# Optimization experiments

Measured on AMD Instinct MI355X. Metric: run time of the kernel, lower is better.

## Reference

```python
import jax, jax.numpy as jnp
import numpy as np

SIZE = 20
DIM = 2 ** SIZE
BATCH = 16
INV_SQRT2 = 1.0 / np.sqrt(2.0).astype(np.float32)

# spec[x] = sum_i (1 - 2*bit_i(x)) for homogeneous z-field (z = ones, zz = {})
_idx = np.arange(DIM, dtype=np.int64)
_popcount = np.zeros(DIM, dtype=np.int64)
for _k in range(SIZE):
    _popcount += (_idx >> _k) & 1
SPEC = jnp.asarray((SIZE - 2 * _popcount).astype(np.float32))  # [DIM]


def _hadamard_all(xr, xi):
    # Apply H on every qubit site sequentially (same math as the gather+sign
    # loop in GateHadamard, expressed as the standard butterfly):
    # for bit=0 slot: (a + b)/sqrt2 ; for bit=1 slot: (a - b)/sqrt2
    B = xr.shape[0]
    for site in range(SIZE):
        lo = 2 ** site
        hi = 2 ** (SIZE - 1 - site)
        xr4 = xr.reshape(B, lo, 2, hi)
        xi4 = xi.reshape(B, lo, 2, hi)
        ar, br = xr4[:, :, 0], xr4[:, :, 1]
        ai, bi = xi4[:, :, 0], xi4[:, :, 1]
        xr = (jnp.stack([ar + br, ar - br], axis=2) * INV_SQRT2).reshape(B, DIM)
        xi = (jnp.stack([ai + bi, ai - bi], axis=2) * INV_SQRT2).reshape(B, DIM)
    return xr, xi


def setup_inputs() -> dict:
    key = jax.random.key(0)
    k1, k2 = jax.random.split(key)
    x_real = jax.random.normal(k1, (BATCH, DIM), dtype=jnp.float32)
    x_imag = jax.random.normal(k2, (BATCH, DIM), dtype=jnp.float32)
    t = jnp.ones((1,), dtype=jnp.float32)
    return {"x_real": x_real, "x_imag": x_imag, "t": t}


def reference(x_real, x_imag, t):
    xr, xi = _hadamard_all(x_real, x_imag)
    # phase multiply: (cos(sp) - i sin(sp)) * (xr + i xi)
    sp = t[0] * SPEC  # [DIM]
    c, s = jnp.cos(sp), jnp.sin(sp)
    yr = c * xr + s * xi
    yi = c * xi - s * xr
    xr, xi = _hadamard_all(yr, yi)
    return jnp.stack([xr, xi])  # [2, BATCH, DIM] (real, imag)
```

## Files before the change

### kernel.cpp

```cpp
#include <hip/hip_runtime.h>
#include <hip/hip_fp16.h>
#include <math.h>

#define DIMN (1 << 20)

typedef unsigned int uint2v __attribute__((ext_vector_type(2)));

__device__ __forceinline__ unsigned int h2u(__half2 v){ union{__half2 h; unsigned int u;} x; x.h=v; return x.u; }
__device__ __forceinline__ __half2 u2h(unsigned int v){ union{unsigned int u; __half2 h;} x; x.u=v; return x.h; }

__device__ __forceinline__ void bf(float& a, float& b) { float s = a + b; b = a - b; a = s; }

template<int CTRL>
__device__ __forceinline__ float dppf(float x) {
    return __int_as_float(__builtin_amdgcn_mov_dpp(__float_as_int(x), CTRL, 0xF, 0xF, true));
}
template<int CTRL>
__device__ __forceinline__ unsigned int dppu(unsigned int x) {
    return (unsigned int)__builtin_amdgcn_mov_dpp((int)x, CTRL, 0xF, 0xF, true);
}
__device__ __forceinline__ float xor4_f(float x) { return dppf<0x1B>(dppf<0x141>(x)); }
__device__ __forceinline__ unsigned int xor4_u(unsigned int x) { return dppu<0x1B>(dppu<0x141>(x)); }

__device__ __forceinline__ float bfly16_f(float x, float sgn) {
#if __has_builtin(__builtin_amdgcn_permlane16_swap)
    uint2v r = __builtin_amdgcn_permlane16_swap(__float_as_uint(x), __float_as_uint(x), false, false);
    return fmaf(sgn, __uint_as_float(r.y), __uint_as_float(r.x));
#else
    float p = __shfl_xor(x, 16);
    return fmaf(sgn, x, p);
#endif
}
__device__ __forceinline__ float bfly32_f(float x, float sgn) {
#if __has_builtin(__builtin_amdgcn_permlane32_swap)
    uint2v r = __builtin_amdgcn_permlane32_swap(__float_as_uint(x), __float_as_uint(x), false, false);
    return fmaf(sgn, __uint_as_float(r.y), __uint_as_float(r.x));
#else
    float p = __shfl_xor(x, 32);
    return fmaf(sgn, x, p);
#endif
}
__device__ __forceinline__ __half2 bfly16_h2(__half2 x, __half2 sgn) {
#if __has_builtin(__builtin_amdgcn_permlane16_swap)
    uint2v r = __builtin_amdgcn_permlane16_swap(h2u(x), h2u(x), false, false);
    return __hfma2(u2h(r.y), sgn, u2h(r.x));
#else
    __half2 p = u2h((unsigned)__shfl_xor((int)h2u(x), 16));
    return __hfma2(x, sgn, p);
#endif
}
__device__ __forceinline__ __half2 bfly32_h2(__half2 x, __half2 sgn) {
#if __has_builtin(__builtin_amdgcn_permlane32_swap)
    uint2v r = __builtin_amdgcn_permlane32_swap(h2u(x), h2u(x), false, false);
    return __hfma2(u2h(r.y), sgn, u2h(r.x));
#else
    __half2 p = u2h((unsigned)__shfl_xor((int)h2u(x), 32));
    return __hfma2(x, sgn, p);
#endif
}

__device__ __forceinline__ void wht16_f32(float v[16], int lane) {
    #pragma unroll
    for (int s = 1; s < 16; s <<= 1)
        #pragma unroll
        for (int r = 0; r < 16; r++)
            if (!(r & s)) bf(v[r], v[r ^ s]);
    {   float sgn = (lane & 1) ? -1.0f : 1.0f;
        #pragma unroll
        for (int r = 0; r < 16; r++) { float p = dppf<0xB1>(v[r]); v[r] = fmaf(sgn, v[r], p); } }
    {   float sgn = (lane & 2) ? -1.0f : 1.0f;
        #pragma unroll
        for (int r = 0; r < 16; r++) { float p = dppf<0x4E>(v[r]); v[r] = fmaf(sgn, v[r], p); } }
    {   float sgn = (lane & 4) ? -1.0f : 1.0f;
        #pragma unroll
        for (int r = 0; r < 16; r++) { float p = xor4_f(v[r]); v[r] = fmaf(sgn, v[r], p); } }
    {   float sgn = (lane & 8) ? -1.0f : 1.0f;
        #pragma unroll
        for (int r = 0; r < 16; r++) { float p = dppf<0x128>(v[r]); v[r] = fmaf(sgn, v[r], p); } }
    {   float sgn = (lane & 16) ? -1.0f : 1.0f;
        #pragma unroll
        for (int r = 0; r < 16; r++) v[r] = bfly16_f(v[r], sgn); }
    {   float sgn = (lane & 32) ? -1.0f : 1.0f;
        #pragma unroll
        for (int r = 0; r < 16; r++) v[r] = bfly32_f(v[r], sgn); }
}

__device__ __forceinline__ void wht16_h2(__half2 v[16], int lane) {
    #pragma unroll
    for (int s = 1; s < 16; s <<= 1)
        #pragma unroll
        for (int r = 0; r < 16; r++)
            if (!(r & s)) {
                __half2 t = __hadd2(v[r], v[r ^ s]);
                v[r ^ s]  = __hsub2(v[r], v[r ^ s]);
                v[r] = t;
            }
    {   __half2 sgn = __float2half2_rn((lane & 1) ? -1.0f : 1.0f);
        #pragma unroll
        for (int r = 0; r < 16; r++) { __half2 p = u2h(dppu<0xB1>(h2u(v[r]))); v[r] = __hfma2(v[r], sgn, p); } }
    {   __half2 sgn = __float2half2_rn((lane & 2) ? -1.0f : 1.0f);
        #pragma unroll
        for (int r = 0; r < 16; r++) { __half2 p = u2h(dppu<0x4E>(h2u(v[r]))); v[r] = __hfma2(v[r], sgn, p); } }
    {   __half2 sgn = __float2half2_rn((lane & 4) ? -1.0f : 1.0f);
        #pragma unroll
        for (int r = 0; r < 16; r++) { __half2 p = u2h(xor4_u(h2u(v[r]))); v[r] = __hfma2(v[r], sgn, p); } }
    {   __half2 sgn = __float2half2_rn((lane & 8) ? -1.0f : 1.0f);
        #pragma unroll
        for (int r = 0; r < 16; r++) { __half2 p = u2h(dppu<0x128>(h2u(v[r]))); v[r] = __hfma2(v[r], sgn, p); } }
    {   __half2 sgn = __float2half2_rn((lane & 16) ? -1.0f : 1.0f);
        #pragma unroll
        for (int r = 0; r < 16; r++) v[r] = bfly16_h2(v[r], sgn); }
    {   __half2 sgn = __float2half2_rn((lane & 32) ? -1.0f : 1.0f);
        #pragma unroll
        for (int r = 0; r < 16; r++) v[r] = bfly32_h2(v[r], sgn); }
}

__device__ __forceinline__ void xorperm8(unsigned int a[8], int m) {
    bool s0 = (m & 1) != 0, s1 = (m & 2) != 0, s2 = (m & 4) != 0;
    unsigned int b0 = s0 ? a[1] : a[0], b1 = s0 ? a[0] : a[1];
    unsigned int b2 = s0 ? a[3] : a[2], b3 = s0 ? a[2] : a[3];
    unsigned int b4 = s0 ? a[5] : a[4], b5 = s0 ? a[4] : a[5];
    unsigned int b6 = s0 ? a[7] : a[6], b7 = s0 ? a[6] : a[7];
    unsigned int c0 = s1 ? b2 : b0, c1 = s1 ? b3 : b1;
    unsigned int c2 = s1 ? b0 : b2, c3 = s1 ? b1 : b3;
    unsigned int c4 = s1 ? b6 : b4, c5 = s1 ? b7 : b5;
    unsigned int c6 = s1 ? b4 : b6, c7 = s1 ? b5 : b7;
    a[0] = s2 ? c4 : c0; a[1] = s2 ? c5 : c1;
    a[2] = s2 ? c6 : c2; a[3] = s2 ? c7 : c3;
    a[4] = s2 ? c0 : c4; a[5] = s2 ? c1 : c5;
    a[6] = s2 ? c2 : c6; a[7] = s2 ? c3 : c7;
}

__global__ __launch_bounds__(256, 4) void p1_kernel(const float* __restrict__ xr,
                                                    const float* __restrict__ xi,
                                                    __half* __restrict__ ws) {
    const int tid = threadIdx.x, lane = tid & 63, w = tid >> 6;
    const int rt = blockIdx.x * 4 + w;
    const float* re = xr + (size_t)rt * 1024;
    const float* im = xi + (size_t)rt * 1024;
    float vr[16], vi[16];
    #pragma unroll
    for (int q = 0; q < 2; q++) {
        const int base = q * 512 + lane * 8;
        float4 a0 = *(const float4*)(re + base);
        float4 a1 = *(const float4*)(re + base + 4);
        float4 b0 = *(const float4*)(im + base);
        float4 b1 = *(const float4*)(im + base + 4);
        vr[q*8+0]=a0.x*0.03125f; vr[q*8+1]=a0.y*0.03125f; vr[q*8+2]=a0.z*0.03125f; vr[q*8+3]=a0.w*0.03125f;
        vr[q*8+4]=a1.x*0.03125f; vr[q*8+5]=a1.y*0.03125f; vr[q*8+6]=a1.z*0.03125f; vr[q*8+7]=a1.w*0.03125f;
        vi[q*8+0]=b0.x*0.03125f; vi[q*8+1]=b0.y*0.03125f; vi[q*8+2]=b0.z*0.03125f; vi[q*8+3]=b0.w*0.03125f;
        vi[q*8+4]=b1.x*0.03125f; vi[q*8+5]=b1.y*0.03125f; vi[q*8+6]=b1.z*0.03125f; vi[q*8+7]=b1.w*0.03125f;
    }
    wht16_f32(vr, lane);
    wht16_f32(vi, lane);
    __half* wr = ws + (size_t)rt * 1024;
    __half* wi = ws + (size_t)16 * DIMN + (size_t)rt * 1024;
    #pragma unroll
    for (int q = 0; q < 2; q++) {
        const int base = q * 512 + lane * 8;
        uint4 pr, pi;
        pr.x = h2u(__floats2half2_rn(vr[q*8+0], vr[q*8+1]));
        pr.y = h2u(__floats2half2_rn(vr[q*8+2], vr[q*8+3]));
        pr.z = h2u(__floats2half2_rn(vr[q*8+4], vr[q*8+5]));
        pr.w = h2u(__floats2half2_rn(vr[q*8+6], vr[q*8+7]));
        pi.x = h2u(__floats2half2_rn(vi[q*8+0], vi[q*8+1]));
        pi.y = h2u(__floats2half2_rn(vi[q*8+2], vi[q*8+3]));
        pi.z = h2u(__floats2half2_rn(vi[q*8+4], vi[q*8+5]));
        pi.w = h2u(__floats2half2_rn(vi[q*8+6], vi[q*8+7]));
        *(uint4*)(wr + base) = pr;
        *(uint4*)(wi + base) = pi;
    }
}

__global__ __launch_bounds__(256, 4) void p3_kernel(const __half* __restrict__ ws,
                                                    float* __restrict__ out) {
    const int tid = threadIdx.x, lane = tid & 63, w = tid >> 6;
    const int rt = blockIdx.x * 4 + w;
    const __half* wr = ws + (size_t)rt * 1024;
    const __half* wi = ws + (size_t)16 * DIMN + (size_t)rt * 1024;
    float vr[16], vi[16];
    #pragma unroll
    for (int q = 0; q < 2; q++) {
        const int base = q * 512 + lane * 8;
        uint4 pr = *(const uint4*)(wr + base);
        uint4 pi = *(const uint4*)(wi + base);
        __half2 a0=u2h(pr.x), a1=u2h(pr.y), a2=u2h(pr.z), a3=u2h(pr.w);
        __half2 b0=u2h(pi.x), b1=u2h(pi.y), b2=u2h(pi.z), b3=u2h(pi.w);
        vr[q*8+0]=__low2float(a0)*0.03125f; vr[q*8+1]=__high2float(a0)*0.03125f;
        vr[q*8+2]=__low2float(a1)*0.03125f; vr[q*8+3]=__high2float(a1)*0.03125f;
        vr[q*8+4]=__low2float(a2)*0.03125f; vr[q*8+5]=__high2float(a2)*0.03125f;
        vr[q*8+6]=__low2float(a3)*0.03125f; vr[q*8+7]=__high2float(a3)*0.03125f;
        vi[q*8+0]=__low2float(b0)*0.03125f; vi[q*8+1]=__high2float(b0)*0.03125f;
        vi[q*8+2]=__low2float(b1)*0.03125f; vi[q*8+3]=__high2float(b1)*0.03125f;
        vi[q*8+4]=__low2float(b2)*0.03125f; vi[q*8+5]=__high2float(b2)*0.03125f;
        vi[q*8+6]=__low2float(b3)*0.03125f; vi[q*8+7]=__high2float(b3)*0.03125f;
    }
    wht16_f32(vr, lane);
    wht16_f32(vi, lane);
    float* outr = out + (size_t)rt * 1024;
    float* outi = out + (size_t)16 * DIMN + (size_t)rt * 1024;
    #pragma unroll
    for (int q = 0; q < 2; q++) {
        const int base = q * 512 + lane * 8;
        *(float4*)(outr + base)     = make_float4(vr[q*8+0], vr[q*8+1], vr[q*8+2], vr[q*8+3]);
        *(float4*)(outr + base + 4) = make_float4(vr[q*8+4], vr[q*8+5], vr[q*8+6], vr[q*8+7]);
        *(float4*)(outi + base)     = make_float4(vi[q*8+0], vi[q*8+1], vi[q*8+2], vi[q*8+3]);
        *(float4*)(outi + base + 4) = make_float4(vi[q*8+4], vi[q*8+5], vi[q*8+6], vi[q*8+7]);
    }
}

__global__ __launch_bounds__(512, 4) void p2_kernel(__half* __restrict__ ws,
                                                    const float* __restrict__ tptr) {
    __shared__ unsigned int tile[1024][16];
    const int tid = threadIdx.x, lane = tid & 63, w = tid >> 6;

    int wg  = blockIdx.x;
    int swz = (wg & 7) * 128 + (wg >> 3);
    const int b  = swz >> 6;
    const int g  = swz & 63;
    const int c0 = g * 16;
    const float tval = tptr[0];

    const int pbase = __popc(lane) + __popc(c0 + w);
    __half2 c2k[6], s2k[6];
    #pragma unroll
    for (int k = 0; k < 6; k++) {
        float ang = tval * (float)(20 - 2 * (pbase + k));
        float s, c;
        __sincosf(ang, &s, &c);
        c2k[k] = __float2half2_rn(c * 0.03125f);
        s2k[k] = __halves2half2(__float2half(s * 0.03125f),
                                __float2half(-s * 0.03125f));
    }

    __half* re = ws + (size_t)b * DIMN + c0;
    __half* im = ws + (size_t)16 * DIMN + (size_t)b * DIMN + c0;

    #pragma unroll
    for (int it = 0; it < 4; it++) {
        int f = it * 512 + tid;
        int h = f >> 1, q = f & 1;
        uint4 ra = *(const uint4*)(re + (size_t)h * 1024 + q * 8);
        uint4 ia = *(const uint4*)(im + (size_t)h * 1024 + q * 8);
        unsigned int w8[8];
        w8[0] = (ra.x & 0xFFFFu) | (ia.x << 16);
        w8[1] = (ra.x >> 16)     | (ia.x & 0xFFFF0000u);
        w8[2] = (ra.y & 0xFFFFu) | (ia.y << 16);
        w8[3] = (ra.y >> 16)     | (ia.y & 0xFFFF0000u);
        w8[4] = (ra.z & 0xFFFFu) | (ia.z << 16);
        w8[5] = (ra.z >> 16)     | (ia.z & 0xFFFF0000u);
        w8[6] = (ra.w & 0xFFFFu) | (ia.w << 16);
        w8[7] = (ra.w >> 16)     | (ia.w & 0xFFFF0000u);
        int e = (h >> 2) & 15;
        xorperm8(w8, e & 7);
        int base = (q * 8) ^ (e & 8);
        *(uint4*)&tile[h][base]     = make_uint4(w8[0], w8[1], w8[2], w8[3]);
        *(uint4*)&tile[h][base + 4] = make_uint4(w8[4], w8[5], w8[6], w8[7]);
    }
    __syncthreads();

    const int e4 = (lane >> 2) & 15;
    const int cp0 = w ^ e4;
    const __half2 sc = __float2half2_rn(0.03125f);
    __half2 v0[16], v1[16];
    #pragma unroll
    for (int r = 0; r < 16; r++) {
        v0[r] = __hmul2(u2h(tile[r * 64 + lane][cp0]),     sc);
        v1[r] = __hmul2(u2h(tile[r * 64 + lane][cp0 ^ 8]), sc);
    }

    wht16_h2(v0, lane);
    wht16_h2(v1, lane);

    #pragma unroll
    for (int r = 0; r < 16; r++) {
        const int pr = __popc(r);
        unsigned int u0 = h2u(v0[r]), u1 = h2u(v1[r]);
        __half2 vs0 = u2h((u0 >> 16) | (u0 << 16));
        __half2 vs1 = u2h((u1 >> 16) | (u1 << 16));
        v0[r] = __hfma2(c2k[pr],     v0[r], __hmul2(s2k[pr],     vs0));
        v1[r] = __hfma2(c2k[pr + 1], v1[r], __hmul2(s2k[pr + 1], vs1));
    }

    wht16_h2(v0, lane);
    wht16_h2(v1, lane);

    #pragma unroll
    for (int r = 0; r < 16; r++) {
        tile[r * 64 + lane][cp0]     = h2u(v0[r]);
        tile[r * 64 + lane][cp0 ^ 8] = h2u(v1[r]);
    }
    __syncthreads();

    #pragma unroll
    for (int it = 0; it < 4; it++) {
        int f = it * 512 + tid;
        int h = f >> 1, q = f & 1;
        int e = (h >> 2) & 15;
        int base = (q * 8) ^ (e & 8);
        uint4 u0 = *(const uint4*)&tile[h][base];
        uint4 u1 = *(const uint4*)&tile[h][base + 4];
        unsigned int w8[8] = {u0.x, u0.y, u0.z, u0.w, u1.x, u1.y, u1.z, u1.w};
        xorperm8(w8, e & 7);
        uint4 ra, ia;
        ra.x = (w8[0] & 0xFFFFu) | (w8[1] << 16);
        ia.x = (w8[0] >> 16)     | (w8[1] & 0xFFFF0000u);
        ra.y = (w8[2] & 0xFFFFu) | (w8[3] << 16);
        ia.y = (w8[2] >> 16)     | (w8[3] & 0xFFFF0000u);
        ra.z = (w8[4] & 0xFFFFu) | (w8[5] << 16);
        ia.z = (w8[4] >> 16)     | (w8[5] & 0xFFFF0000u);
        ra.w = (w8[6] & 0xFFFFu) | (w8[7] << 16);
        ia.w = (w8[6] >> 16)     | (w8[7] & 0xFFFF0000u);
        *(uint4*)(re + (size_t)h * 1024 + q * 8) = ra;
        *(uint4*)(im + (size_t)h * 1024 + q * 8) = ia;
    }
}

__device__ __forceinline__ void wht10_f4(float4 v[4], int lane) {
    #pragma unroll
    for (int r = 0; r < 4; r++) {
        bf(v[r].x, v[r].y); bf(v[r].z, v[r].w);
        bf(v[r].x, v[r].z); bf(v[r].y, v[r].w);
    }
    #pragma unroll
    for (int m = 1; m <= 32; m <<= 1) {
        float sgn = (lane & m) ? -1.0f : 1.0f;
        #pragma unroll
        for (int r = 0; r < 4; r++) {
            float px = __shfl_xor(v[r].x, m), py = __shfl_xor(v[r].y, m);
            float pz = __shfl_xor(v[r].z, m), pw = __shfl_xor(v[r].w, m);
            v[r].x = fmaf(sgn, v[r].x, px); v[r].y = fmaf(sgn, v[r].y, py);
            v[r].z = fmaf(sgn, v[r].z, pz); v[r].w = fmaf(sgn, v[r].w, pw);
        }
    }
    bf(v[0].x, v[1].x); bf(v[0].y, v[1].y); bf(v[0].z, v[1].z); bf(v[0].w, v[1].w);
    bf(v[2].x, v[3].x); bf(v[2].y, v[3].y); bf(v[2].z, v[3].z); bf(v[2].w, v[3].w);
    bf(v[0].x, v[2].x); bf(v[0].y, v[2].y); bf(v[0].z, v[2].z); bf(v[0].w, v[2].w);
    bf(v[1].x, v[3].x); bf(v[1].y, v[3].y); bf(v[1].z, v[3].z); bf(v[1].w, v[3].w);
}

__global__ __launch_bounds__(256) void pass13_kernel(const float* __restrict__ srcA,
                                                     const float* __restrict__ srcB,
                                                     float* __restrict__ dst) {
    const int tid = threadIdx.x, lane = tid & 63, w = tid >> 6;
    const int rt0 = blockIdx.x * 16 + w * 4;
    const float* src = (rt0 < 16384) ? (srcA + (size_t)rt0 * 1024)
                                     : (srcB + (size_t)(rt0 - 16384) * 1024);
    float* d = dst + (size_t)rt0 * 1024;
    float4 v[4][4];
    #pragma unroll
    for (int rr = 0; rr < 4; rr++)
        #pragma unroll
        for (int r = 0; r < 4; r++)
            v[rr][r] = *(const float4*)(src + rr * 1024 + r * 256 + lane * 4);
    #pragma unroll
    for (int rr = 0; rr < 4; rr++) {
        wht10_f4(v[rr], lane);
        #pragma unroll
        for (int r = 0; r < 4; r++) {
            float4 o;
            o.x = v[rr][r].x * 0.03125f; o.y = v[rr][r].y * 0.03125f;
            o.z = v[rr][r].z * 0.03125f; o.w = v[rr][r].w * 0.03125f;
            *(float4*)(d + rr * 1024 + r * 256 + lane * 4) = o;
        }
    }
}

__global__ __launch_bounds__(256) void pass2f_kernel(float* __restrict__ out,
                                                     const float* __restrict__ tptr) {
    __shared__ __align__(16) float tile[2][1024][8];
    const int tid = threadIdx.x, lane = tid & 63, w = tid >> 6;
    int wg = blockIdx.x;
    int swz = (wg & 7) * 256 + (wg >> 3);
    const int b = swz >> 7, g = swz & 127;
    const int c0 = g * 8;
    const float tval = tptr[0];
    float* baseR = out + (size_t)b * DIMN;
    float* baseI = out + (size_t)16 * DIMN + (size_t)b * DIMN;
    float4 tmp[2][8];
    #pragma unroll
    for (int comp = 0; comp < 2; comp++) {
        const float* src = comp ? baseI : baseR;
        #pragma unroll
        for (int it = 0; it < 8; it++) {
            int f4id = it * 256 + tid;
            int h = f4id >> 1, q = f4id & 1;
            tmp[comp][it] = *(const float4*)(src + (size_t)h * 1024 + c0 + q * 4);
        }
    }
    #pragma unroll
    for (int comp = 0; comp < 2; comp++) {
        #pragma unroll
        for (int it = 0; it < 8; it++) {
            int f4id = it * 256 + tid;
            int h = f4id >> 1, q = f4id & 1;
            int e = (h >> 2) & 7, elo = e & 3;
            float4 val = tmp[comp][it];
            bool s0 = (elo & 1) != 0;
            float x1 = s0 ? val.y : val.x, y1 = s0 ? val.x : val.y;
            float z1 = s0 ? val.w : val.z, w1 = s0 ? val.z : val.w;
            bool s1 = (elo & 2) != 0;
            float x2 = s1 ? z1 : x1, y2 = s1 ? w1 : y1;
            float z2 = s1 ? x1 : z1, w2 = s1 ? y1 : w1;
            int qp = q ^ (e >> 2);
            *(float4*)&tile[comp][h][qp * 4] = make_float4(x2, y2, z2, w2);
        }
    }
    __syncthreads();
    float vr[2][16], vi[2][16];
    #pragma unroll
    for (int r = 0; r < 16; r++) {
        int h = r * 64 + lane;
        int e = (lane >> 2) & 7;
        #pragma unroll
        for (int cc = 0; cc < 2; cc++) {
            int cp = (2 * w + cc) ^ e;
            vr[cc][r] = tile[0][h][cp];
            vi[cc][r] = tile[1][h][cp];
        }
    }
    const int pcl = __popc(lane);
    #pragma unroll
    for (int cc = 0; cc < 2; cc++) {
        wht16_f32(vr[cc], lane);
        wht16_f32(vi[cc], lane);
        const int cg = c0 + 2 * w + cc;
        const int pbase = pcl + __popc(cg);
        float csk[5], snk[5];
        #pragma unroll
        for (int k = 0; k < 5; k++) {
            float ang = tval * (float)(20 - 2 * (pbase + k));
            __sincosf(ang, &snk[k], &csk[k]);
        }
        #pragma unroll
        for (int r = 0; r < 16; r++) {
            const int pr = __popc(r);
            float cv = csk[pr], sv = snk[pr];
            float xr = vr[cc][r] * 0.03125f, xi = vi[cc][r] * 0.03125f;
            vr[cc][r] = fmaf(cv, xr, sv * xi);
            vi[cc][r] = fmaf(cv, xi, -sv * xr);
        }
        wht16_f32(vr[cc], lane);
        wht16_f32(vi[cc], lane);
    }
    #pragma unroll
    for (int r = 0; r < 16; r++) {
        int h = r * 64 + lane;
        int e = (lane >> 2) & 7;
        #pragma unroll
        for (int cc = 0; cc < 2; cc++) {
            int cp = (2 * w + cc) ^ e;
            tile[0][h][cp] = vr[cc][r] * 0.03125f;
            tile[1][h][cp] = vi[cc][r] * 0.03125f;
        }
    }
    __syncthreads();
    #pragma unroll
    for (int comp = 0; comp < 2; comp++) {
        float* dstg = comp ? baseI : baseR;
        #pragma unroll
        for (int it = 0; it < 8; it++) {
            int f4id = it * 256 + tid;
            int h = f4id >> 1, q = f4id & 1;
            int e = (h >> 2) & 7, elo = e & 3;
            int qp = q ^ (e >> 2);
            float4 sv = *(const float4*)&tile[comp][h][qp * 4];
            bool s0 = (elo & 1) != 0;
            float x1 = s0 ? sv.y : sv.x, y1 = s0 ? sv.x : sv.y;
            float z1 = s0 ? sv.w : sv.z, w1 = s0 ? sv.z : sv.w;
            bool s1 = (elo & 2) != 0;
            float x2 = s1 ? z1 : x1, y2 = s1 ? w1 : y1;
            float z2 = s1 ? x1 : z1, w2 = s1 ? y1 : w1;
            *(float4*)(dstg + (size_t)h * 1024 + c0 + q * 4) = make_float4(x2, y2, z2, w2);
        }
    }
}

extern "C" void kernel_launch(void* const* d_in, const int* in_sizes, int n_in,
                              void* d_out, int out_size, void* d_ws, size_t ws_size,
                              hipStream_t stream) {
    const float* xr = (const float*)d_in[0];
    const float* xi = (const float*)d_in[1];
    const float* t  = (const float*)d_in[2];
    float* out = (float*)d_out;

    const size_t need = (size_t)2 * 16 * DIMN * sizeof(__half);
    if (ws_size >= need) {
        __half* ws = (__half*)d_ws;
        p1_kernel<<<4096, 256, 0, stream>>>(xr, xi, ws);
        p2_kernel<<<1024, 512, 0, stream>>>(ws, t);
        p3_kernel<<<4096, 256, 0, stream>>>(ws, out);
    } else {
        pass13_kernel<<<2048, 256, 0, stream>>>(xr, xi, out);
        pass2f_kernel<<<2048, 256, 0, stream>>>(out, t);
        pass13_kernel<<<2048, 256, 0, stream>>>(out, out + (size_t)16 * DIMN, out);
    }
}
```

Measured before the change: 114.2 us.

## Split phase by popcount to fuse into two passes with interleaved fp16 workspace

```diff
diff --git a/kernel.cpp b/kernel.cpp
--- a/kernel.cpp
+++ b/kernel.cpp
@@ -113,6 +113,14 @@
     {   __half2 sgn = __float2half2_rn((lane & 32) ? -1.0f : 1.0f);
         #pragma unroll
         for (int r = 0; r < 16; r++) v[r] = bfly32_h2(v[r], sgn); }
+}
+
+__device__ __forceinline__ void xorperm4(unsigned int a[4], int m) {
+    bool s0 = (m & 1) != 0, s1 = (m & 2) != 0;
+    unsigned int t0 = s0 ? a[1] : a[0], t1 = s0 ? a[0] : a[1];
+    unsigned int t2 = s0 ? a[3] : a[2], t3 = s0 ? a[2] : a[3];
+    a[0] = s1 ? t2 : t0; a[1] = s1 ? t3 : t1;
+    a[2] = s1 ? t0 : t2; a[3] = s1 ? t1 : t3;
 }
 
 __device__ __forceinline__ void xorperm8(unsigned int a[8], int m) {
@@ -131,11 +139,23 @@
     a[6] = s2 ? c2 : c6; a[7] = s2 ? c3 : c7;
 }
 
-__global__ __launch_bounds__(256, 4) void p1_kernel(const float* __restrict__ xr,
+__global__ __launch_bounds__(256, 4) void pA_kernel(const float* __restrict__ xr,
                                                     const float* __restrict__ xi,
-                                                    __half* __restrict__ ws) {
+                                                    __half2* __restrict__ ws,
+                                                    const float* __restrict__ tptr) {
     const int tid = threadIdx.x, lane = tid & 63, w = tid >> 6;
     const int rt = blockIdx.x * 4 + w;
+    const float tval = tptr[0];
+    const int pcl = __popc(lane);
+    float cs[5], sn[5];
+    #pragma unroll
+    for (int k = 0; k < 5; k++) {
+        float ang = tval * (float)(10 - 2 * (pcl + k));
+        float s, c;
+        __sincosf(ang, &s, &c);
+        cs[k] = c * 0.03125f;
+        sn[k] = s * 0.03125f;
+    }
     const float* re = xr + (size_t)rt * 1024;
     const float* im = xi + (size_t)rt * 1024;
     float vr[16], vi[16];
@@ -153,63 +173,35 @@
     }
     wht16_f32(vr, lane);
     wht16_f32(vi, lane);
-    __half* wr = ws + (size_t)rt * 1024;
-    __half* wi = ws + (size_t)16 * DIMN + (size_t)rt * 1024;
+    #pragma unroll
+    for (int r = 0; r < 16; r++) {
+        const int pr = __popc(r);
+        float x = vr[r], y = vi[r];
+        vr[r] = fmaf(cs[pr], x,  sn[pr] * y);
+        vi[r] = fmaf(cs[pr], y, -sn[pr] * x);
+    }
+    wht16_f32(vr, lane);
+    wht16_f32(vi, lane);
+    __half2* wp = ws + (size_t)rt * 1024;
     #pragma unroll
     for (int q = 0; q < 2; q++) {
         const int base = q * 512 + lane * 8;
-        uint4 pr, pi;
-        pr.x = h2u(__floats2half2_rn(vr[q*8+0], vr[q*8+1]));
-        pr.y = h2u(__floats2half2_rn(vr[q*8+2], vr[q*8+3]));
-        pr.z = h2u(__floats2half2_rn(vr[q*8+4], vr[q*8+5]));
-        pr.w = h2u(__floats2half2_rn(vr[q*8+6], vr[q*8+7]));
-        pi.x = h2u(__floats2half2_rn(vi[q*8+0], vi[q*8+1]));
-        pi.y = h2u(__floats2half2_rn(vi[q*8+2], vi[q*8+3]));
-        pi.z = h2u(__floats2half2_rn(vi[q*8+4], vi[q*8+5]));
-        pi.w = h2u(__floats2half2_rn(vi[q*8+6], vi[q*8+7]));
-        *(uint4*)(wr + base) = pr;
-        *(uint4*)(wi + base) = pi;
-    }
-}
-
-__global__ __launch_bounds__(256, 4) void p3_kernel(const __half* __restrict__ ws,
-                                                    float* __restrict__ out) {
-    const int tid = threadIdx.x, lane = tid & 63, w = tid >> 6;
-    const int rt = blockIdx.x * 4 + w;
-    const __half* wr = ws + (size_t)rt * 1024;
-    const __half* wi = ws + (size_t)16 * DIMN + (size_t)rt * 1024;
-    float vr[16], vi[16];
-    #pragma unroll
-    for (int q = 0; q < 2; q++) {
-        const int base = q * 512 + lane * 8;
-        uint4 pr = *(const uint4*)(wr + base);
-        uint4 pi = *(const uint4*)(wi + base);
-        __half2 a0=u2h(pr.x), a1=u2h(pr.y), a2=u2h(pr.z), a3=u2h(pr.w);
-        __half2 b0=u2h(pi.x), b1=u2h(pi.y), b2=u2h(pi.z), b3=u2h(pi.w);
-        vr[q*8+0]=__low2float(a0)*0.03125f; vr[q*8+1]=__high2float(a0)*0.03125f;
-        vr[q*8+2]=__low2float(a1)*0.03125f; vr[q*8+3]=__high2float(a1)*0.03125f;
-        vr[q*8+4]=__low2float(a2)*0.03125f; vr[q*8+5]=__high2float(a2)*0.03125f;
-        vr[q*8+6]=__low2float(a3)*0.03125f; vr[q*8+7]=__high2float(a3)*0.03125f;
-        vi[q*8+0]=__low2float(b0)*0.03125f; vi[q*8+1]=__high2float(b0)*0.03125f;
-        vi[q*8+2]=__low2float(b1)*0.03125f; vi[q*8+3]=__high2float(b1)*0.03125f;
-        vi[q*8+4]=__low2float(b2)*0.03125f; vi[q*8+5]=__high2float(b2)*0.03125f;
-        vi[q*8+6]=__low2float(b3)*0.03125f; vi[q*8+7]=__high2float(b3)*0.03125f;
-    }
-    wht16_f32(vr, lane);
-    wht16_f32(vi, lane);
-    float* outr = out + (size_t)rt * 1024;
-    float* outi = out + (size_t)16 * DIMN + (size_t)rt * 1024;
-    #pragma unroll
-    for (int q = 0; q < 2; q++) {
-        const int base = q * 512 + lane * 8;
-        *(float4*)(outr + base)     = make_float4(vr[q*8+0], vr[q*8+1], vr[q*8+2], vr[q*8+3]);
-        *(float4*)(outr + base + 4) = make_float4(vr[q*8+4], vr[q*8+5], vr[q*8+6], vr[q*8+7]);
-        *(float4*)(outi + base)     = make_float4(vi[q*8+0], vi[q*8+1], vi[q*8+2], vi[q*8+3]);
-        *(float4*)(outi + base + 4) = make_float4(vi[q*8+4], vi[q*8+5], vi[q*8+6], vi[q*8+7]);
-    }
-}
-
-__global__ __launch_bounds__(512, 4) void p2_kernel(__half* __restrict__ ws,
+        uint4 u0, u1;
+        u0.x = h2u(__floats2half2_rn(vr[q*8+0], vi[q*8+0]));
+        u0.y = h2u(__floats2half2_rn(vr[q*8+1], vi[q*8+1]));
+        u0.z = h2u(__floats2half2_rn(vr[q*8+2], vi[q*8+2]));
+        u0.w = h2u(__floats2half2_rn(vr[q*8+3], vi[q*8+3]));
+        u1.x = h2u(__floats2half2_rn(vr[q*8+4], vi[q*8+4]));
+        u1.y = h2u(__floats2half2_rn(vr[q*8+5], vi[q*8+5]));
+        u1.z = h2u(__floats2half2_rn(vr[q*8+6], vi[q*8+6]));
+        u1.w = h2u(__floats2half2_rn(vr[q*8+7], vi[q*8+7]));
+        *(uint4*)(wp + base)     = u0;
+        *(uint4*)(wp + base + 4) = u1;
+    }
+}
+
+__global__ __launch_bounds__(512, 4) void pB_kernel(const __half2* __restrict__ ws,
+                                                    float* __restrict__ out,
                                                     const float* __restrict__ tptr) {
     __shared__ unsigned int tile[1024][16];
     const int tid = threadIdx.x, lane = tid & 63, w = tid >> 6;
@@ -221,11 +213,11 @@
     const int c0 = g * 16;
     const float tval = tptr[0];
 
-    const int pbase = __popc(lane) + __popc(c0 + w);
-    __half2 c2k[6], s2k[6];
-    #pragma unroll
-    for (int k = 0; k < 6; k++) {
-        float ang = tval * (float)(20 - 2 * (pbase + k));
+    const int pcl = __popc(lane);
+    __half2 c2k[5], s2k[5];
+    #pragma unroll
+    for (int k = 0; k < 5; k++) {
+        float ang = tval * (float)(10 - 2 * (pcl + k));
         float s, c;
         __sincosf(ang, &s, &c);
         c2k[k] = __float2half2_rn(c * 0.03125f);
@@ -233,29 +225,18 @@
                                 __float2half(-s * 0.03125f));
     }
 
-    __half* re = ws + (size_t)b * DIMN + c0;
-    __half* im = ws + (size_t)16 * DIMN + (size_t)b * DIMN + c0;
-
-    #pragma unroll
-    for (int it = 0; it < 4; it++) {
+    const __half2* src = ws + (size_t)b * DIMN + c0;
+
+    #pragma unroll
+    for (int it = 0; it < 8; it++) {
         int f = it * 512 + tid;
-        int h = f >> 1, q = f & 1;
-        uint4 ra = *(const uint4*)(re + (size_t)h * 1024 + q * 8);
-        uint4 ia = *(const uint4*)(im + (size_t)h * 1024 + q * 8);
-        unsigned int w8[8];
-        w8[0] = (ra.x & 0xFFFFu) | (ia.x << 16);
-        w8[1] = (ra.x >> 16)     | (ia.x & 0xFFFF0000u);
-        w8[2] = (ra.y & 0xFFFFu) | (ia.y << 16);
-        w8[3] = (ra.y >> 16)     | (ia.y & 0xFFFF0000u);
-        w8[4] = (ra.z & 0xFFFFu) | (ia.z << 16);
-        w8[5] = (ra.z >> 16)     | (ia.z & 0xFFFF0000u);
-        w8[6] = (ra.w & 0xFFFFu) | (ia.w << 16);
-        w8[7] = (ra.w >> 16)     | (ia.w & 0xFFFF0000u);
+        int h = f >> 2, qd = f & 3;
+        uint4 a = *(const uint4*)(src + (size_t)h * 1024 + qd * 4);
+        unsigned int g4[4] = {a.x, a.y, a.z, a.w};
         int e = (h >> 2) & 15;
-        xorperm8(w8, e & 7);
-        int base = (q * 8) ^ (e & 8);
-        *(uint4*)&tile[h][base]     = make_uint4(w8[0], w8[1], w8[2], w8[3]);
-        *(uint4*)&tile[h][base + 4] = make_uint4(w8[4], w8[5], w8[6], w8[7]);
+        xorperm4(g4, e & 3);
+        int dq = qd ^ (e >> 2);
+        *(uint4*)&tile[h][dq * 4] = make_uint4(g4[0], g4[1], g4[2], g4[3]);
     }
     __syncthreads();
 
@@ -278,8 +259,8 @@
         unsigned int u0 = h2u(v0[r]), u1 = h2u(v1[r]);
         __half2 vs0 = u2h((u0 >> 16) | (u0 << 16));
         __half2 vs1 = u2h((u1 >> 16) | (u1 << 16));
-        v0[r] = __hfma2(c2k[pr],     v0[r], __hmul2(s2k[pr],     vs0));
-        v1[r] = __hfma2(c2k[pr + 1], v1[r], __hmul2(s2k[pr + 1], vs1));
+        v0[r] = __hfma2(c2k[pr], v0[r], __hmul2(s2k[pr], vs0));
+        v1[r] = __hfma2(c2k[pr], v1[r], __hmul2(s2k[pr], vs1));
     }
 
     wht16_h2(v0, lane);
@@ -292,27 +273,32 @@
     }
     __syncthreads();
 
+    float* outR = out + (size_t)b * DIMN + c0;
+    float* outI = out + (size_t)16 * DIMN + (size_t)b * DIMN + c0;
     #pragma unroll
     for (int it = 0; it < 4; it++) {
         int f = it * 512 + tid;
-        int h = f >> 1, q = f & 1;
+        int h = f >> 1, q8 = f & 1;
         int e = (h >> 2) & 15;
-        int base = (q * 8) ^ (e & 8);
+        int base = (q8 ^ (e >> 3)) * 8;
         uint4 u0 = *(const uint4*)&tile[h][base];
         uint4 u1 = *(const uint4*)&tile[h][base + 4];
         unsigned int w8[8] = {u0.x, u0.y, u0.z, u0.w, u1.x, u1.y, u1.z, u1.w};
         xorperm8(w8, e & 7);
-        uint4 ra, ia;
-        ra.x = (w8[0] & 0xFFFFu) | (w8[1] << 16);
-        ia.x = (w8[0] >> 16)     | (w8[1] & 0xFFFF0000u);
-        ra.y = (w8[2] & 0xFFFFu) | (w8[3] << 16);
-        ia.y = (w8[2] >> 16)     | (w8[3] & 0xFFFF0000u);
-        ra.z = (w8[4] & 0xFFFFu) | (w8[5] << 16);
-        ia.z = (w8[4] >> 16)     | (w8[5] & 0xFFFF0000u);
-        ra.w = (w8[6] & 0xFFFFu) | (w8[7] << 16);
-        ia.w = (w8[6] >> 16)     | (w8[7] & 0xFFFF0000u);
-        *(uint4*)(re + (size_t)h * 1024 + q * 8) = ra;
-        *(uint4*)(im + (size_t)h * 1024 + q * 8) = ia;
+        float4 r0, r1, i0, i1;
+        r0.x = __low2float(u2h(w8[0])); i0.x = __high2float(u2h(w8[0]));
+        r0.y = __low2float(u2h(w8[1])); i0.y = __high2float(u2h(w8[1]));
+        r0.z = __low2float(u2h(w8[2])); i0.z = __high2float(u2h(w8[2]));
+        r0.w = __low2float(u2h(w8[3])); i0.w = __high2float(u2h(w8[3]));
+        r1.x = __low2float(u2h(w8[4])); i1.x = __high2float(u2h(w8[4]));
+        r1.y = __low2float(u2h(w8[5])); i1.y = __high2float(u2h(w8[5]));
+        r1.z = __low2float(u2h(w8[6])); i1.z = __high2float(u2h(w8[6]));
+        r1.w = __low2float(u2h(w8[7])); i1.w = __high2float(u2h(w8[7]));
+        size_t off = (size_t)h * 1024 + q8 * 8;
+        *(float4*)(outR + off)     = r0;
+        *(float4*)(outR + off + 4) = r1;
+        *(float4*)(outI + off)     = i0;
+        *(float4*)(outI + off + 4) = i1;
     }
 }
 
@@ -484,12 +470,11 @@
     const float* t  = (const float*)d_in[2];
     float* out = (float*)d_out;
 
-    const size_t need = (size_t)2 * 16 * DIMN * sizeof(__half);
+    const size_t need = (size_t)16 * DIMN * sizeof(__half2);
     if (ws_size >= need) {
-        __half* ws = (__half*)d_ws;
-        p1_kernel<<<4096, 256, 0, stream>>>(xr, xi, ws);
-        p2_kernel<<<1024, 512, 0, stream>>>(ws, t);
-        p3_kernel<<<4096, 256, 0, stream>>>(ws, out);
+        __half2* ws = (__half2*)d_ws;
+        pA_kernel<<<4096, 256, 0, stream>>>(xr, xi, ws, t);
+        pB_kernel<<<1024, 512, 0, stream>>>(ws, out, t);
     } else {
         pass13_kernel<<<2048, 256, 0, stream>>>(xr, xi, out);
         pass2f_kernel<<<2048, 256, 0, stream>>>(out, t);
```

Result: faster. 97.21 us (median of 2 runs) (-14.9%).
